# Kernel tuning notes

Measured on AMD Instinct MI355X. Metric: run time of the kernel, lower is better.

## Reference

```python
import jax, jax.numpy as jnp
import numpy as np

N = 50000
E = 800000
NFEAT = 128
NHID = 64
NCLASS = 40


def setup_inputs() -> dict:
    key = jax.random.key(0)
    ks = jax.random.split(key, 12)
    return {
        "x": jax.random.normal(ks[0], (N, NFEAT), dtype=jnp.float32),
        "M": jax.random.uniform(ks[1], (N, 1), dtype=jnp.float32),
        "AM": jax.random.uniform(ks[2], (N, 1), dtype=jnp.float32),
        "adj_vals": jax.random.uniform(ks[3], (E,), dtype=jnp.float32),
        "adjZ_vals": jax.random.uniform(ks[4], (E,), dtype=jnp.float32),
        "W0": jax.random.normal(ks[5], (NFEAT, NFEAT), dtype=jnp.float32) * (1.414 / np.sqrt(NFEAT)),
        "b0": jnp.zeros((NFEAT,), dtype=jnp.float32),
        "W1": jax.random.normal(ks[6], (NFEAT, NHID), dtype=jnp.float32) * (1.414 / np.sqrt(NFEAT)),
        "b1": jnp.zeros((NHID,), dtype=jnp.float32),
        "W2": jax.random.normal(ks[7], (NHID, NCLASS), dtype=jnp.float32) * (1.0 / np.sqrt(NHID)),
        "b2": jnp.zeros((NCLASS,), dtype=jnp.float32),
        "row": jax.random.randint(ks[8], (E,), 0, N, dtype=jnp.int32),
        "col": jax.random.randint(ks[9], (E,), 0, N, dtype=jnp.int32),
    }


def _spmm(vals, row, col, X, n):
    # sparse (COO) @ dense: out[r] = sum_e vals[e] * X[col[e]] for row[e]==r
    return jax.ops.segment_sum(vals[:, None] * X[col], row, num_segments=n)


def reference(x, M, AM, adj_vals, adjZ_vals, W0, b0, W1, b1, W2, b2, row, col):
    n = x.shape[0]
    # gc0: PaGConv(nfeat->nfeat) on adjZ, then ReLU (dropout is identity in eval)
    h = _spmm(adjZ_vals, row, col, M * x, n) * AM
    h = jax.nn.relu(h @ W0 + b0)
    # gc1: PaGConv(nfeat->nhid) on adjZ, then ReLU
    h = _spmm(adjZ_vals, row, col, M * h, n) * AM
    h = jax.nn.relu(h @ W1 + b1)
    # gc2: plain GConv(nhid->nclass) on adj
    h = _spmm(adj_vals, row, col, h, n)
    h = h @ W2 + b2
    return jax.nn.log_softmax(h, axis=1)
```

## Files before the change

### kernel.cpp

```cpp
#include <hip/hip_runtime.h>
#include <hip/hip_bf16.h>
#include <math.h>


typedef __attribute__((ext_vector_type(8))) short bf16x8;
typedef __attribute__((ext_vector_type(4))) float f32x4;

__device__ __forceinline__ float rl_f(float v, int j) {
    return __builtin_bit_cast(float,
        __builtin_amdgcn_readlane(__builtin_bit_cast(int, v), j));
}
__device__ __forceinline__ int rl_i(int v, int j) {
    return __builtin_amdgcn_readlane(v, j);
}
__device__ __forceinline__ unsigned short f2bf(float f) {
    unsigned u = __builtin_bit_cast(unsigned, f);
    u += 0x7fffu + ((u >> 16) & 1u);
    return (unsigned short)(u >> 16);
}
__device__ __forceinline__ unsigned pack2bf(float lo, float hi) {
    return (unsigned)f2bf(lo) | ((unsigned)f2bf(hi) << 16);
}
__device__ __forceinline__ float bf_lo(unsigned u) {
    return __builtin_bit_cast(float, u << 16);
}
__device__ __forceinline__ float bf_hi(unsigned u) {
    return __builtin_bit_cast(float, u & 0xffff0000u);
}
__device__ __forceinline__ float clampf(float v) {
    return fminf(fmaxf(v, -1e30f), 1e30f);
}


__global__ void prep_wt(const float* __restrict__ W0, const float* __restrict__ W1,
                        const float* __restrict__ W2,
                        unsigned short* __restrict__ wt0, unsigned short* __restrict__ wt1,
                        unsigned short* __restrict__ wt2) {
    int idx = blockIdx.x * 256 + threadIdx.x;
    if (idx < 128 * 128) {
        int nn = idx >> 7, k = idx & 127;
        wt0[idx] = f2bf(W0[k * 128 + nn]);
    }
    idx -= 128 * 128;
    if (idx >= 0 && idx < 64 * 128) {
        int nn = idx >> 7, k = idx & 127;
        wt1[idx] = f2bf(W1[k * 64 + nn]);
    }
    idx -= 64 * 128;
    if (idx >= 0 && idx < 48 * 64) {
        int nn = idx >> 6, k = idx & 63;
        wt2[idx] = (nn < 40) ? f2bf(W2[k * 40 + nn]) : (unsigned short)0;
    }
}


template <int K, int COLS, int NTPAD, bool ABF16, bool MSCALE>
__device__ __forceinline__ void gemm_mfma_body(const void* __restrict__ Asrc,
                                               const float* __restrict__ Mv,
                                               const unsigned short* __restrict__ Wt,
                                               unsigned short* __restrict__ outp,
                                               int n, int bid) {
    constexpr int KS = K / 32;
    const int lane = threadIdx.x & 63;
    const int wid = threadIdx.x >> 6;
    const int m15 = lane & 15;
    const int q = lane >> 4;
    const int rA = bid * 64 + wid * 16 + m15;

    bf16x8 a[KS];
    if constexpr (ABF16) {
        const unsigned short* A = (const unsigned short*)Asrc;
#pragma unroll
        for (int ks = 0; ks < KS; ++ks) {
            uint4 z = make_uint4(0u, 0u, 0u, 0u);
            if (rA < n) z = *(const uint4*)(A + (size_t)rA * K + ks * 32 + q * 8);
            a[ks] = __builtin_bit_cast(bf16x8, z);
        }
    } else {
        const float* A = (const float*)Asrc;
        float m = 1.0f;
        if constexpr (MSCALE) { if (rA < n) m = Mv[rA]; }
#pragma unroll
        for (int ks = 0; ks < KS; ++ks) {
            float4 lo = make_float4(0.f, 0.f, 0.f, 0.f);
            float4 hi = make_float4(0.f, 0.f, 0.f, 0.f);
            if (rA < n) {
                lo = *(const float4*)(A + (size_t)rA * K + ks * 32 + q * 8);
                hi = *(const float4*)(A + (size_t)rA * K + ks * 32 + q * 8 + 4);
            }
            union { bf16x8 v; unsigned short u[8]; } pk;
            pk.u[0] = f2bf(lo.x * m); pk.u[1] = f2bf(lo.y * m);
            pk.u[2] = f2bf(lo.z * m); pk.u[3] = f2bf(lo.w * m);
            pk.u[4] = f2bf(hi.x * m); pk.u[5] = f2bf(hi.y * m);
            pk.u[6] = f2bf(hi.z * m); pk.u[7] = f2bf(hi.w * m);
            a[ks] = pk.v;
        }
    }

#pragma unroll
    for (int nt = 0; nt < NTPAD / 16; ++nt) {
        f32x4 acc = {0.f, 0.f, 0.f, 0.f};
        const int bn = nt * 16 + m15;
#pragma unroll
        for (int ks = 0; ks < KS; ++ks) {
            const uint4 z = *(const uint4*)(Wt + (size_t)bn * K + ks * 32 + q * 8);
            const bf16x8 b = __builtin_bit_cast(bf16x8, z);
            acc = __builtin_amdgcn_mfma_f32_16x16x32_bf16(a[ks], b, acc, 0, 0, 0);
        }
        const int gc = nt * 16 + m15;
#pragma unroll
        for (int rr = 0; rr < 4; ++rr) {
            const int gr = bid * 64 + wid * 16 + q * 4 + rr;
            bool ok = gr < n;
            if constexpr (NTPAD != COLS) ok = ok && (gc < COLS);
            if (ok) outp[(size_t)gr * COLS + gc] = f2bf(clampf(acc[rr]));
        }
    }
}

template <int K, int COLS, int NTPAD, bool ABF16, bool MSCALE>
__launch_bounds__(256)
__global__ void gemm_mfma(const void* __restrict__ A, const float* __restrict__ Mv,
                          const unsigned short* __restrict__ Wt,
                          unsigned short* __restrict__ out, int n) {
    gemm_mfma_body<K, COLS, NTPAD, ABF16, MSCALE>(A, Mv, Wt, out, n, blockIdx.x);
}


__launch_bounds__(256)
__global__ void gemm0_hist(const float* __restrict__ x, const float* __restrict__ Mv,
                           const unsigned short* __restrict__ Wt0,
                           unsigned short* __restrict__ t_buf,
                           const int* __restrict__ row, int* __restrict__ cnt,
                           int* __restrict__ pos_local, int n, int E, int gemmBlocks) {
    const int b = blockIdx.x;
    if (b < gemmBlocks) {
        gemm_mfma_body<128, 128, 128, false, true>(x, Mv, Wt0, t_buf, n, b);
    } else {
        const int e = (b - gemmBlocks) * 256 + threadIdx.x;
        if (e < E) pos_local[e] = atomicAdd(&cnt[row[e]], 1);
    }
}


__global__ void scan_part(const int* __restrict__ cnt, int* __restrict__ out,
                          int* __restrict__ bsums, int n) {
    __shared__ int sdata[256];
    const int t = threadIdx.x;
    const int base = blockIdx.x * 1024 + t * 4;
    int v[4];
#pragma unroll
    for (int i = 0; i < 4; ++i) v[i] = (base + i < n) ? cnt[base + i] : 0;
    int tsum = v[0] + v[1] + v[2] + v[3];
    sdata[t] = tsum;
    __syncthreads();
    for (int off = 1; off < 256; off <<= 1) {
        int x = (t >= off) ? sdata[t - off] : 0;
        __syncthreads();
        sdata[t] += x;
        __syncthreads();
    }
    int run = sdata[t] - tsum;
    if (t == 255) bsums[blockIdx.x] = sdata[t];
#pragma unroll
    for (int i = 0; i < 4; ++i) {
        if (base + i < n) out[base + i] = run;
        run += v[i];
    }
}

__global__ void scan_top(int* __restrict__ bs, int nb) {
    int t = threadIdx.x;
    int orig = (t < nb) ? bs[t] : 0;
    int v = orig;
#pragma unroll
    for (int off = 1; off < 64; off <<= 1) {
        int x = __shfl_up(v, off);
        if (t >= off) v += x;
    }
    if (t < nb) bs[t] = v - orig;
}

__global__ void scan_add(int* __restrict__ rp, const int* __restrict__ bs,
                         int n, int total) {
    int i = blockIdx.x * blockDim.x + threadIdx.x;
    if (i < n) rp[i] += bs[i >> 10];
    if (i == 0) rp[n] = total;
}


__global__ void scatter_kernel(const int* __restrict__ row, const int* __restrict__ col,
                               const float* __restrict__ vA, const float* __restrict__ vZ,
                               const int* __restrict__ rp, const int* __restrict__ pos_local,
                               float* __restrict__ packed, int E) {
    int e = blockIdx.x * blockDim.x + threadIdx.x;
    if (e >= E) return;
    const int pos = rp[row[e]] + pos_local[e];
    float3 pk;
    pk.x = __int_as_float(col[e]);
    pk.y = vZ[e];
    pk.z = vA[e];
    *(float3*)&packed[(size_t)3 * pos] = pk;
}


__launch_bounds__(256)
__global__ void spmm128_kernel(const float* __restrict__ packed,
                               const int* __restrict__ rp, const unsigned short* __restrict__ X,
                               const float* __restrict__ AM, const float* __restrict__ Mv,
                               const float* __restrict__ bias,
                               unsigned short* __restrict__ out, int n) {
    const int lane = threadIdx.x & 63;
    const int r = (int)((blockIdx.x * (unsigned)blockDim.x + threadIdx.x) >> 6);
    if (r >= n) return;
    const int s = __builtin_amdgcn_readfirstlane(rp[r]);
    const int e = __builtin_amdgcn_readfirstlane(rp[r + 1]);

    float acc0 = 0.0f, acc1 = 0.0f;
    for (int base = s; base < e; base += 64) {
        const int nn = min(64, e - base);
        int ci = 0; float vf = 0.0f;
        if (lane < nn) {
            const float3 pk = *(const float3*)&packed[(size_t)3 * (base + lane)];
            ci = __builtin_bit_cast(int, pk.x);
            vf = pk.y;
        }
        int j = 0;
        for (; j + 8 <= nn; j += 8) {
            unsigned u[8];
#pragma unroll
            for (int q = 0; q < 8; ++q) {
                const int cq = rl_i(ci, j + q);
                u[q] = *(const unsigned*)(X + (size_t)cq * 128 + lane * 2);
            }
#pragma unroll
            for (int q = 0; q < 8; ++q) {
                const float vq = rl_f(vf, j + q);
                acc0 += vq * bf_lo(u[q]);
                acc1 += vq * bf_hi(u[q]);
            }
        }
        for (; j < nn; ++j) {
            const int cq = rl_i(ci, j);
            const float vq = rl_f(vf, j);
            const unsigned u = *(const unsigned*)(X + (size_t)cq * 128 + lane * 2);
            acc0 += vq * bf_lo(u);
            acc1 += vq * bf_hi(u);
        }
    }

    const float am = AM[r];
    const float mr = Mv[r];
    const float o0 = fminf(fmaxf((acc0 * am + bias[2 * lane]) * mr, 0.0f), 1e30f);
    const float o1 = fminf(fmaxf((acc1 * am + bias[2 * lane + 1]) * mr, 0.0f), 1e30f);
    ((unsigned*)out)[(size_t)r * 64 + lane] = pack2bf(o0, o1);
}


__launch_bounds__(256)
__global__ void spmm64_kernel(const float* __restrict__ packed,
                              const int* __restrict__ rp, const unsigned short* __restrict__ X,
                              const float* __restrict__ AM, const float* __restrict__ bias,
                              unsigned short* __restrict__ out, int n) {
    const int lane = threadIdx.x & 63;
    const int g = lane >> 5;
    const int ls = lane & 31;
    const int r = (int)((blockIdx.x * (unsigned)blockDim.x + threadIdx.x) >> 6);
    if (r >= n) return;
    const int s = __builtin_amdgcn_readfirstlane(rp[r]);
    const int e = __builtin_amdgcn_readfirstlane(rp[r + 1]);

    float acc0 = 0.0f, acc1 = 0.0f;
    for (int base = s; base < e; base += 64) {
        const int nn = min(64, e - base);
        int ci = 0; float vf = 0.0f;
        if (lane < nn) {
            const float3 pk = *(const float3*)&packed[(size_t)3 * (base + lane)];
            ci = __builtin_bit_cast(int, pk.x);
            vf = pk.y;
        }
        for (int j = 0; j < nn; j += 8) {
#pragma unroll
            for (int q = 0; q < 4; ++q) {
                const int jj = j + 2 * q + g;
                const bool ok = jj < nn;
                const int idx = jj & 63;
                const int c = __shfl(ci, idx);
                const float v = __shfl(vf, idx);
                if (ok) {
                    const unsigned u = *(const unsigned*)(X + (size_t)c * 64 + ls * 2);
                    acc0 += v * bf_lo(u);
                    acc1 += v * bf_hi(u);
                }
            }
        }
    }
    acc0 += __shfl_xor(acc0, 32);
    acc1 += __shfl_xor(acc1, 32);

    if (lane < 32) {
        const float am = AM[r];
        const float o0 = fminf(fmaxf(acc0 * am + bias[2 * ls], 0.0f), 1e30f);
        const float o1 = fminf(fmaxf(acc1 * am + bias[2 * ls + 1], 0.0f), 1e30f);
        ((unsigned*)out)[(size_t)r * 32 + ls] = pack2bf(o0, o1);
    }
}


__launch_bounds__(256)
__global__ void spmm40_kernel(const float* __restrict__ packed,
                              const int* __restrict__ rp, const unsigned short* __restrict__ X,
                              const float* __restrict__ bias,
                              float* __restrict__ out, int n) {
    const int lane = threadIdx.x & 63;
    const int g = lane / 20;
    const int ls = lane - 20 * g;
    const bool active = g < 3;
    const int r = (int)((blockIdx.x * (unsigned)blockDim.x + threadIdx.x) >> 6);
    if (r >= n) return;
    const int s = __builtin_amdgcn_readfirstlane(rp[r]);
    const int e = __builtin_amdgcn_readfirstlane(rp[r + 1]);

    float acc0 = 0.0f, acc1 = 0.0f;
    for (int base = s; base < e; base += 64) {
        const int nn = min(64, e - base);
        int ci = 0; float vf = 0.0f;
        if (lane < nn) {
            const float3 pk = *(const float3*)&packed[(size_t)3 * (base + lane)];
            ci = __builtin_bit_cast(int, pk.x);
            vf = pk.z;
        }
        for (int j = 0; j < nn; j += 12) {
#pragma unroll
            for (int q = 0; q < 4; ++q) {
                const int jj = j + 3 * q + g;
                const bool ok = active && jj < nn;
                const int idx = jj & 63;
                const int c = __shfl(ci, idx);
                const float v = __shfl(vf, idx);
                if (ok) {
                    const unsigned u = *(const unsigned*)(X + (size_t)c * 40 + ls * 2);
                    acc0 += v * bf_lo(u);
                    acc1 += v * bf_hi(u);
                }
            }
        }
    }
    {
        const float a1 = __shfl(acc0, (lane + 20) & 63);
        const float a2 = __shfl(acc0, (lane + 40) & 63);
        const float b1 = __shfl(acc1, (lane + 20) & 63);
        const float b2 = __shfl(acc1, (lane + 40) & 63);
        acc0 += a1 + a2;
        acc1 += b1 + b2;
    }

    const bool own = lane < 20;
    const float vv0 = own ? fminf(fmaxf(acc0 + bias[2 * ls], -1e30f), 1e30f) : -INFINITY;
    const float vv1 = own ? fminf(fmaxf(acc1 + bias[2 * ls + 1], -1e30f), 1e30f) : -INFINITY;
    float mx = fmaxf(vv0, vv1);
#pragma unroll
    for (int off = 32; off > 0; off >>= 1) mx = fmaxf(mx, __shfl_xor(mx, off));
    float sum = own ? (expf(vv0 - mx) + expf(vv1 - mx)) : 0.0f;
#pragma unroll
    for (int off = 32; off > 0; off >>= 1) sum += __shfl_xor(sum, off);
    if (own) {
        const float lse = mx + logf(sum);
        *(float2*)(out + (size_t)r * 40 + ls * 2) = make_float2(vv0 - lse, vv1 - lse);
    }
}


extern "C" void kernel_launch(void* const* d_in, const int* in_sizes, int n_in,
                              void* d_out, int out_size, void* d_ws, size_t ws_size,
                              hipStream_t stream) {
    const float* x    = (const float*)d_in[0];
    const float* M    = (const float*)d_in[1];
    const float* AM   = (const float*)d_in[2];
    const float* adjv = (const float*)d_in[3];
    const float* adjZ = (const float*)d_in[4];
    const float* W0   = (const float*)d_in[5];
    const float* b0   = (const float*)d_in[6];
    const float* W1   = (const float*)d_in[7];
    const float* b1   = (const float*)d_in[8];
    const float* W2   = (const float*)d_in[9];
    const float* b2   = (const float*)d_in[10];
    const int* row    = (const int*)d_in[11];
    const int* col    = (const int*)d_in[12];
    float* out = (float*)d_out;

    const int n = in_sizes[1];
    const int E = in_sizes[3];

    float* t_f   = (float*)d_ws;
    unsigned short* t_buf = (unsigned short*)t_f;
    unsigned short* wt0 = t_buf + (size_t)n * 128;
    unsigned short* wt1 = wt0 + 128 * 128;
    unsigned short* wt2 = wt1 + 64 * 128;
    float* h_f   = t_f + (size_t)n * 128;
    unsigned short* h_buf = (unsigned short*)h_f;
    int* cnt     = (int*)(h_f + (size_t)n * 128);
    int* rp      = cnt + n;
    int* bsums   = rp + (n + 1);
    float* packed = (float*)(bsums + 64);
    int* pos_local = (int*)h_f;

    hipMemsetAsync(cnt, 0, (size_t)n * sizeof(int), stream);
    prep_wt<<<(128 * 128 + 64 * 128 + 48 * 64 + 255) / 256, 256, 0, stream>>>(
        W0, W1, W2, wt0, wt1, wt2);

    const int gemm0Blocks = (n + 63) / 64;
    const int histBlocks  = (E + 255) / 256;
    gemm0_hist<<<gemm0Blocks + histBlocks, 256, 0, stream>>>(x, M, wt0, t_buf, row, cnt,
                                                             pos_local, n, E, gemm0Blocks);

    const int nblk = (n + 1023) >> 10;
    scan_part<<<nblk, 256, 0, stream>>>(cnt, rp, bsums, n);
    scan_top<<<1, 64, 0, stream>>>(bsums, nblk);
    scan_add<<<(n + 255) / 256, 256, 0, stream>>>(rp, bsums, n, E);
    scatter_kernel<<<(E + 255) / 256, 256, 0, stream>>>(row, col, adjv, adjZ, rp,
                                                        pos_local, packed, E);

    const int spmmBlocks = (n + 3) / 4;
    const int gemmBlocks = (n + 63) / 64;

    spmm128_kernel<<<spmmBlocks, 256, 0, stream>>>(packed, rp, t_buf, AM, M, b0, h_buf, n);
    gemm_mfma<128, 64, 64, true, false><<<gemmBlocks, 256, 0, stream>>>(h_buf, nullptr, wt1,
                                                                        t_buf, n);
    spmm64_kernel<<<spmmBlocks, 256, 0, stream>>>(packed, rp, t_buf, AM, b1, h_buf, n);
    gemm_mfma<64, 40, 48, true, false><<<gemmBlocks, 256, 0, stream>>>(h_buf, nullptr, wt2,
                                                                       t_buf, n);
    spmm40_kernel<<<spmmBlocks, 256, 0, stream>>>(packed, rp, t_buf, b2, out, n);
}
```

Baseline: 287.9 us.

## Replace global atomic row histogram with per-block LDS histograms and column scan

```diff
diff --git a/kernel.cpp b/kernel.cpp
--- a/kernel.cpp
+++ b/kernel.cpp
@@ -5,6 +5,10 @@
 
 typedef __attribute__((ext_vector_type(8))) short bf16x8;
 typedef __attribute__((ext_vector_type(4))) float f32x4;
+
+#define HIST_EPB_LOG 14
+#define HIST_EPB 16384
+#define NBINS 50176
 
 __device__ __forceinline__ float rl_f(float v, int j) {
     return __builtin_bit_cast(float,
@@ -59,10 +63,10 @@
                                                const float* __restrict__ Mv,
                                                const unsigned short* __restrict__ Wt,
                                                unsigned short* __restrict__ outp,
-                                               int n, int bid) {
+                                               int n, int bid, int tid) {
     constexpr int KS = K / 32;
-    const int lane = threadIdx.x & 63;
-    const int wid = threadIdx.x >> 6;
+    const int lane = tid & 63;
+    const int wid = tid >> 6;
     const int m15 = lane & 15;
     const int q = lane >> 4;
     const int rA = bid * 64 + wid * 16 + m15;
@@ -123,48 +127,74 @@
 __global__ void gemm_mfma(const void* __restrict__ A, const float* __restrict__ Mv,
                           const unsigned short* __restrict__ Wt,
                           unsigned short* __restrict__ out, int n) {
-    gemm_mfma_body<K, COLS, NTPAD, ABF16, MSCALE>(A, Mv, Wt, out, n, blockIdx.x);
-}
-
-
-__launch_bounds__(256)
-__global__ void gemm0_hist(const float* __restrict__ x, const float* __restrict__ Mv,
+    gemm_mfma_body<K, COLS, NTPAD, ABF16, MSCALE>(A, Mv, Wt, out, n, blockIdx.x,
+                                                  threadIdx.x);
+}
+
+
+__launch_bounds__(1024)
+__global__ void hist_gemm0(const int* __restrict__ row,
+                           unsigned short* __restrict__ cntmat,
+                           unsigned short* __restrict__ lrank, int E, int NB,
+                           const float* __restrict__ x, const float* __restrict__ Mv,
                            const unsigned short* __restrict__ Wt0,
-                           unsigned short* __restrict__ t_buf,
-                           const int* __restrict__ row, int* __restrict__ cnt,
-                           int* __restrict__ pos_local, int n, int E, int gemmBlocks) {
-    const int b = blockIdx.x;
-    if (b < gemmBlocks) {
-        gemm_mfma_body<128, 128, 128, false, true>(x, Mv, Wt0, t_buf, n, b);
+                           unsigned short* __restrict__ t_buf, int n) {
+    __shared__ unsigned hcnt[NBINS / 2];
+    const int blk = blockIdx.x;
+    const int t = threadIdx.x;
+    if (blk < NB) {
+        for (int i = t; i < NBINS / 2; i += 1024) hcnt[i] = 0u;
+        __syncthreads();
+        const int s = blk << HIST_EPB_LOG;
+        const int e = min(E, s + HIST_EPB);
+        for (int i = s + t; i < e; i += 1024) {
+            const int r = row[i];
+            const unsigned sh = (unsigned)(r & 1) << 4;
+            const unsigned old = atomicAdd(&hcnt[r >> 1], 1u << sh);
+            lrank[i] = (unsigned short)((old >> sh) & 0xffffu);
+        }
+        __syncthreads();
+        unsigned* dst = (unsigned*)(cntmat + (size_t)blk * NBINS);
+        for (int i = t; i < NBINS / 2; i += 1024) dst[i] = hcnt[i];
     } else {
-        const int e = (b - gemmBlocks) * 256 + threadIdx.x;
-        if (e < E) pos_local[e] = atomicAdd(&cnt[row[e]], 1);
-    }
-}
-
-
-__global__ void scan_part(const int* __restrict__ cnt, int* __restrict__ out,
-                          int* __restrict__ bsums, int n) {
+        const int sub = t >> 8;
+        gemm_mfma_body<128, 128, 128, false, true>(x, Mv, Wt0, t_buf, n,
+                                                   (blk - NB) * 4 + sub, t & 255);
+    }
+}
+
+
+__global__ void scan_part2(unsigned short* __restrict__ cm, int* __restrict__ rp,
+                           int* __restrict__ bsums, int n, int NB) {
     __shared__ int sdata[256];
     const int t = threadIdx.x;
     const int base = blockIdx.x * 1024 + t * 4;
-    int v[4];
-#pragma unroll
-    for (int i = 0; i < 4; ++i) v[i] = (base + i < n) ? cnt[base + i] : 0;
-    int tsum = v[0] + v[1] + v[2] + v[3];
+    unsigned r0 = 0, r1 = 0, r2 = 0, r3 = 0;
+    for (int b = 0; b < NB; ++b) {
+        uint2* p = (uint2*)&cm[(size_t)b * NBINS + base];
+        const uint2 c = *p;
+        uint2 o;
+        o.x = r0 | (r1 << 16);
+        o.y = r2 | (r3 << 16);
+        *p = o;
+        r0 += c.x & 0xffffu; r1 += c.x >> 16;
+        r2 += c.y & 0xffffu; r3 += c.y >> 16;
+    }
+    int v[4] = {(int)r0, (int)r1, (int)r2, (int)r3};
+    const int tsum = v[0] + v[1] + v[2] + v[3];
     sdata[t] = tsum;
     __syncthreads();
     for (int off = 1; off < 256; off <<= 1) {
-        int x = (t >= off) ? sdata[t - off] : 0;
+        int xv = (t >= off) ? sdata[t - off] : 0;
         __syncthreads();
-        sdata[t] += x;
+        sdata[t] += xv;
         __syncthreads();
     }
     int run = sdata[t] - tsum;
     if (t == 255) bsums[blockIdx.x] = sdata[t];
 #pragma unroll
     for (int i = 0; i < 4; ++i) {
-        if (base + i < n) out[base + i] = run;
+        if (base + i < n) rp[base + i] = run;
         run += v[i];
     }
 }
@@ -191,11 +221,15 @@
 
 __global__ void scatter_kernel(const int* __restrict__ row, const int* __restrict__ col,
                                const float* __restrict__ vA, const float* __restrict__ vZ,
-                               const int* __restrict__ rp, const int* __restrict__ pos_local,
+                               const int* __restrict__ rp,
+                               const unsigned short* __restrict__ cm,
+                               const unsigned short* __restrict__ lrank,
                                float* __restrict__ packed, int E) {
     int e = blockIdx.x * blockDim.x + threadIdx.x;
     if (e >= E) return;
-    const int pos = rp[row[e]] + pos_local[e];
+    const int r = row[e];
+    const int pos = rp[r] + (int)cm[(size_t)(e >> HIST_EPB_LOG) * NBINS + r]
+                          + (int)lrank[e];
     float3 pk;
     pk.x = __int_as_float(col[e]);
     pk.y = vZ[e];
@@ -399,30 +433,30 @@
     unsigned short* wt2 = wt1 + 64 * 128;
     float* h_f   = t_f + (size_t)n * 128;
     unsigned short* h_buf = (unsigned short*)h_f;
-    int* cnt     = (int*)(h_f + (size_t)n * 128);
-    int* rp      = cnt + n;
+    unsigned short* lrank  = (unsigned short*)h_f;
+    unsigned short* cntmat = lrank + (size_t)E;
+    int* rp      = (int*)(h_f + (size_t)n * 128);
     int* bsums   = rp + (n + 1);
     float* packed = (float*)(bsums + 64);
-    int* pos_local = (int*)h_f;
-
-    hipMemsetAsync(cnt, 0, (size_t)n * sizeof(int), stream);
+
+    const int NB = (E + HIST_EPB - 1) >> HIST_EPB_LOG;
+    const int gemmBlocks = (n + 63) / 64;
+    const int gemmB4 = (gemmBlocks + 3) / 4;
+
     prep_wt<<<(128 * 128 + 64 * 128 + 48 * 64 + 255) / 256, 256, 0, stream>>>(
         W0, W1, W2, wt0, wt1, wt2);
 
-    const int gemm0Blocks = (n + 63) / 64;
-    const int histBlocks  = (E + 255) / 256;
-    gemm0_hist<<<gemm0Blocks + histBlocks, 256, 0, stream>>>(x, M, wt0, t_buf, row, cnt,
-                                                             pos_local, n, E, gemm0Blocks);
+    hist_gemm0<<<NB + gemmB4, 1024, 0, stream>>>(row, cntmat, lrank, E, NB,
+                                                 x, M, wt0, t_buf, n);
 
     const int nblk = (n + 1023) >> 10;
-    scan_part<<<nblk, 256, 0, stream>>>(cnt, rp, bsums, n);
+    scan_part2<<<nblk, 256, 0, stream>>>(cntmat, rp, bsums, n, NB);
     scan_top<<<1, 64, 0, stream>>>(bsums, nblk);
     scan_add<<<(n + 255) / 256, 256, 0, stream>>>(rp, bsums, n, E);
     scatter_kernel<<<(E + 255) / 256, 256, 0, stream>>>(row, col, adjv, adjZ, rp,
-                                                        pos_local, packed, E);
+                                                        cntmat, lrank, packed, E);
 
     const int spmmBlocks = (n + 3) / 4;
-    const int gemmBlocks = (n + 63) / 64;
 
     spmm128_kernel<<<spmmBlocks, 256, 0, stream>>>(packed, rp, t_buf, AM, M, b0, h_buf, n);
     gemm_mfma<128, 64, 64, true, false><<<gemmBlocks, 256, 0, stream>>>(h_buf, nullptr, wt1,
```

New measurement: 273.9 us. 1.05x faster.
